# Kernel tuning notes

Hardware: AMD Instinct MI355X
Metric: run time of the kernel (lower is better)

## Reference

```python
import jax, jax.numpy as jnp
import numpy as np
import math

D_MODEL = 512
N_HEAD = 8
HEAD_DIM = D_MODEL // N_HEAD


def _rel_sinusoid(seq_len, dim):
    # Sinusoidal embedding for relative positions -seq_len .. seq_len-1, shape [2L, dim]
    half = dim // 2
    inv_freq = jnp.exp(jnp.arange(half, dtype=jnp.float32) * (-math.log(10000.0) / (half - 1)))
    ang = jnp.arange(-seq_len, seq_len, dtype=jnp.float32)[:, None] * inv_freq[None, :]
    return jnp.concatenate([jnp.sin(ang), jnp.cos(ang)], axis=1)  # [2L, dim]


def _shift(BD):
    # Transformer-XL shift trick: [b, n, L, 2L] -> [b, n, L, L]
    b, n, L, _ = BD.shape
    BD = jnp.concatenate([BD, jnp.zeros((b, n, L, 1), BD.dtype)], axis=-1)  # [b,n,L,2L+1]
    BD = BD.reshape(b, n, -1, L)[:, :, :-1].reshape(b, n, L, -1)  # [b,n,L,2L]
    return BD[:, :, :, L:]


def setup_inputs() -> dict:
    key = jax.random.key(0)
    ks = jax.random.split(key, 6)
    B, L = 8, 1024
    x = jax.random.normal(ks[0], (B, L, D_MODEL), jnp.float32)
    mask = jax.random.randint(ks[1], (B, L), 0, 2).astype(jnp.int32)
    W_qkv = jax.random.normal(ks[2], (D_MODEL, 3 * D_MODEL), jnp.float32) / math.sqrt(D_MODEL)
    r_r_bias = jax.random.normal(ks[3], (N_HEAD, HEAD_DIM), jnp.float32) * 0.1
    r_w_bias = jax.random.normal(ks[4], (N_HEAD, HEAD_DIM), jnp.float32) * 0.1
    w_kr = jax.random.normal(ks[5], (HEAD_DIM, HEAD_DIM), jnp.float32) * 0.1
    return {"x": x, "mask": mask, "W_qkv": W_qkv, "r_r_bias": r_r_bias, "r_w_bias": r_w_bias, "w_kr": w_kr}


def reference(x, mask, W_qkv, r_r_bias, r_w_bias, w_kr):
    B, L, d_model = x.shape
    scale = math.sqrt(HEAD_DIM)
    pos_embed = _rel_sinusoid(L, HEAD_DIM)  # [2L, head_dim]

    qkv = x @ W_qkv  # [B, L, 3*d_model]
    q, k, v = jnp.split(qkv, 3, axis=-1)
    q = q.reshape(B, L, N_HEAD, HEAD_DIM).transpose(0, 2, 1, 3)  # [B, H, L, hd]
    k = k.reshape(B, L, N_HEAD, HEAD_DIM).transpose(0, 2, 1, 3)
    v = v.reshape(B, L, N_HEAD, HEAD_DIM).transpose(0, 2, 1, 3)

    rw_head_q = q + r_r_bias[None, :, None, :]
    AC = jnp.einsum('bnqd,bnkd->bnqk', rw_head_q, k)  # [B,H,L,L]

    rel = pos_embed @ w_kr  # [2L, hd]
    D_ = jnp.einsum('nd,ld->nl', r_w_bias, rel)[None, :, None, :]  # [1,H,1,2L]
    B_ = jnp.einsum('bnqd,ld->bnql', q, rel)  # [B,H,L,2L]
    BD = _shift(B_ + D_)  # [B,H,L,L]

    attn = (AC + BD) / scale
    attn = jnp.where(mask[:, None, None, :] == 0, jnp.float32(1e-9), attn)
    attn = jax.nn.softmax(attn, axis=-1)  # dropout is identity at eval

    out = jnp.einsum('bnqk,bnkd->bnqd', attn, v)  # [B,H,L,hd]
    return out.transpose(0, 2, 1, 3).reshape(B, L, d_model)
```

## Files before the change

kernel.cpp:

```cpp
#include <hip/hip_runtime.h>
#include <hip/hip_bf16.h>
#include <stdint.h>

typedef __bf16 bf16x8 __attribute__((ext_vector_type(8)));
typedef float  f32x4  __attribute__((ext_vector_type(4)));

#define D_MODEL 512
#define N_HEAD  8
#define HD      64
#define L_      1024
#define SCALE   0.125f
#define EXP_NEG8 3.35462628e-4f
#define L2E     1.44269504f
#define NEG8L2E -11.54156036f

__device__ __forceinline__ unsigned short f2bf(float f) {
  unsigned int u = __builtin_bit_cast(unsigned int, f);
  u += 0x7FFFu + ((u >> 16) & 1u);
  return (unsigned short)(u >> 16);
}
__device__ __forceinline__ float bf2f(unsigned short h) {
  unsigned int u = ((unsigned int)h) << 16;
  return __builtin_bit_cast(float, u);
}

__device__ __forceinline__ void gld_lds16(const void* g, void* l) {
  __builtin_amdgcn_global_load_lds(
      (const __attribute__((address_space(1))) void*)g,
      (__attribute__((address_space(3))) void*)l, 16, 0, 0);
}
__device__ __forceinline__ void gld_lds4(const void* g, void* l) {
  __builtin_amdgcn_global_load_lds(
      (const __attribute__((address_space(1))) void*)g,
      (__attribute__((address_space(3))) void*)l, 4, 0, 0);
}

__global__ __launch_bounds__(256) void k_cvt_x(const float* __restrict__ x,
                                               unsigned short* __restrict__ xbf) {
  int t = blockIdx.x * 256 + threadIdx.x;
  const float4* p = reinterpret_cast<const float4*>(x) + (size_t)t * 2;
  float4 a = p[0], b = p[1];
  ushort4 o0 = { f2bf(a.x), f2bf(a.y), f2bf(a.z), f2bf(a.w) };
  ushort4 o1 = { f2bf(b.x), f2bf(b.y), f2bf(b.z), f2bf(b.w) };
  ushort4* q = reinterpret_cast<ushort4*>(xbf) + (size_t)t * 2;
  q[0] = o0; q[1] = o1;
}

__global__ __launch_bounds__(256) void k_cvt_wt(const float* __restrict__ W,
                                                unsigned short* __restrict__ Wt) {
  __shared__ float tile[32][33];
  int kb = blockIdx.x;
  int nb = blockIdx.y;
  int t = threadIdx.x;
  int r = t >> 3, c4 = (t & 7) * 4;
  float4 v = *reinterpret_cast<const float4*>(W + (size_t)(kb * 32 + r) * 1536 + nb * 32 + c4);
  tile[r][c4 + 0] = v.x; tile[r][c4 + 1] = v.y; tile[r][c4 + 2] = v.z; tile[r][c4 + 3] = v.w;
  __syncthreads();
  int a = t >> 3, b4 = (t & 7) * 4;
  ushort4 o = { f2bf(tile[b4 + 0][a]), f2bf(tile[b4 + 1][a]),
                f2bf(tile[b4 + 2][a]), f2bf(tile[b4 + 3][a]) };
  *reinterpret_cast<ushort4*>(Wt + (size_t)(nb * 32 + a) * 512 + kb * 32 + b4) = o;
}

__global__ __launch_bounds__(256) void k_stab(float* __restrict__ SCF,
                                              unsigned short* __restrict__ SBF) {
  int tid = blockIdx.x * 256 + threadIdx.x;
  int l = tid >> 6, d = tid & 63;
  const float kInv = -9.210340371976184f / 31.0f;
  float f = expf((float)(d & 31) * kInv);
  float ang = (float)l * f;
  float v = (d < 32) ? sinf(ang) : cosf(ang);
  SCF[tid] = v;
  SBF[tid] = f2bf(v);
}

__global__ __launch_bounds__(256) void k_wz(const unsigned short* __restrict__ Wt,
                                            const float* __restrict__ wkr,
                                            const float* __restrict__ rwb,
                                            unsigned short* __restrict__ Wzt,
                                            float* __restrict__ CZ) {
  __shared__ float wkrS[64][64];
  __shared__ float panS[64][36];
  int blk = blockIdx.x;
  int h = blk >> 4, kc = blk & 15;
  int t = threadIdx.x;
  for (int i = t; i < 4096; i += 256) wkrS[i >> 6][i & 63] = wkr[i];
  {
    int d = t >> 2, j0 = (t & 3) * 8;
    const unsigned short* src = Wt + (size_t)(h * 64 + d) * 512 + kc * 32 + j0;
    for (int j = 0; j < 8; ++j) panS[d][j0 + j] = bf2f(src[j]);
  }
  __syncthreads();
  int e = t >> 2, j0 = (t & 3) * 8;
  float acc[8];
  for (int j = 0; j < 8; ++j) acc[j] = 0.f;
  for (int d = 0; d < 64; ++d) {
    float wv = wkrS[e][d];
    for (int j = 0; j < 8; ++j) acc[j] += wv * panS[d][j0 + j];
  }
  unsigned short* dst = Wzt + (size_t)(h * 64 + e) * 512 + kc * 32 + j0;
  ushort4 o0 = { f2bf(acc[0]), f2bf(acc[1]), f2bf(acc[2]), f2bf(acc[3]) };
  ushort4 o1 = { f2bf(acc[4]), f2bf(acc[5]), f2bf(acc[6]), f2bf(acc[7]) };
  *reinterpret_cast<ushort4*>(dst) = o0;
  *reinterpret_cast<ushort4*>(dst + 4) = o1;
  if (kc == 0 && t < 64) {
    float c = 0.f;
    for (int d = 0; d < 64; ++d) c += wkrS[t][d] * rwb[h * 64 + d];
    CZ[h * 64 + t] = c;
  }
}

__global__ __launch_bounds__(256, 3) void k_gemm_qkv(const unsigned short* __restrict__ Xbf,
                                                     const unsigned short* __restrict__ Wt,
                                                     const float* __restrict__ rrb,
                                                     const float* __restrict__ SCF,
                                                     const float* __restrict__ CZ,
                                                     unsigned short* __restrict__ QKV,
                                                     unsigned short* __restrict__ Vt,
                                                     unsigned short* __restrict__ Aq) {
  __shared__ unsigned short As[2][128][32];
  __shared__ unsigned short Bs[2][128][32];
  int lin = blockIdx.y * 64 + blockIdx.x;
  int xcd = lin & 7, idx = lin >> 3;
  int bx = xcd * 8 + idx / 16;
  int by = idx % 16;
  int m0 = bx * 128;
  int n0 = by * 128;
  int w = threadIdx.x >> 6, lane = threadIdx.x & 63;
  int lr = lane & 15, g = lane >> 4;
  int wm = (w >> 1) * 64, wn = (w & 1) * 64;
  int srow = lane >> 2, schk = (lane & 3) * 8;

  auto stage = [&](int buf, int k0) {
#pragma unroll
    for (int j = 0; j < 2; ++j) {
      int row = w * 32 + j * 16 + srow;
      gld_lds16(Xbf + (size_t)(m0 + row) * 512 + k0 + schk, &As[buf][w * 32 + j * 16][0]);
      gld_lds16(Wt  + (size_t)(n0 + row) * 512 + k0 + schk, &Bs[buf][w * 32 + j * 16][0]);
    }
  };

  f32x4 acc[4][4];
  for (int i = 0; i < 4; ++i) for (int j = 0; j < 4; ++j) acc[i][j] = (f32x4){0.f, 0.f, 0.f, 0.f};

  stage(0, 0);
  __syncthreads();

  for (int it = 0; it < 16; ++it) {
    int cur = it & 1;
    if (it < 15) stage(cur ^ 1, (it + 1) * 32);
    bf16x8 a[4], b[4];
#pragma unroll
    for (int mt = 0; mt < 4; ++mt)
      a[mt] = __builtin_bit_cast(bf16x8, *reinterpret_cast<const uint4*>(&As[cur][wm + mt * 16 + lr][g * 8]));
#pragma unroll
    for (int nt = 0; nt < 4; ++nt)
      b[nt] = __builtin_bit_cast(bf16x8, *reinterpret_cast<const uint4*>(&Bs[cur][wn + nt * 16 + lr][g * 8]));
#pragma unroll
    for (int mt = 0; mt < 4; ++mt)
#pragma unroll
      for (int nt = 0; nt < 4; ++nt)
        acc[mt][nt] = __builtin_amdgcn_mfma_f32_16x16x32_bf16(a[mt], b[nt], acc[mt][nt], 0, 0, 0);
    __syncthreads();
  }

  int region = n0 >> 9;
  if (region == 3) {
    int nvb = (n0 - 1536) + wn;
    int h = nvb >> 6;
    int bb = m0 >> 10;
    float cz0 = CZ[nvb + lr];
    float cz1 = CZ[nvb + 16 + lr];
    float cz2 = CZ[nvb + 32 + lr];
    float cz3 = CZ[nvb + 48 + lr];
#pragma unroll
    for (int mt = 0; mt < 4; ++mt)
#pragma unroll
      for (int r = 0; r < 4; ++r) {
        int m = m0 + wm + mt * 16 + g * 4 + r;
        int lrow = m & 1023;
        const float* sc = SCF + (size_t)lrow * 64;
        float s0 = sc[lr], s1 = sc[16 + lr], c0 = sc[32 + lr], c1 = sc[48 + lr];
        float z0 = acc[mt][0][r] + cz0;
        float z1 = acc[mt][1][r] + cz1;
        float z2 = acc[mt][2][r] + cz2;
        float z3 = acc[mt][3][r] + cz3;
        unsigned short* ap = Aq + ((size_t)(bb * 8 + h) * 1024 + lrow) * 64;
        ap[lr]      = f2bf((z0 * c0 + z2 * s0) * SCALE);
        ap[16 + lr] = f2bf((z1 * c1 + z3 * s1) * SCALE);
        ap[32 + lr] = f2bf((z2 * c0 - z0 * s0) * SCALE);
        ap[48 + lr] = f2bf((z3 * c1 - z1 * s1) * SCALE);
      }
  } else if (region == 2) {
#pragma unroll
    for (int mt = 0; mt < 4; ++mt)
#pragma unroll
      for (int nt = 0; nt < 4; ++nt) {
        int m = m0 + wm + mt * 16 + g * 4;
        int n = n0 + wn + nt * 16 + lr;
        int nv = n - 1024;
        int bb = m >> 10, h = nv >> 6, d = nv & 63;
        ushort4 o = { f2bf(acc[mt][nt][0]), f2bf(acc[mt][nt][1]),
                      f2bf(acc[mt][nt][2]), f2bf(acc[mt][nt][3]) };
        *reinterpret_cast<ushort4*>(Vt + (size_t)((bb * 8 + h) * 64 + d) * 1024 + (m & 1023)) = o;
      }
  } else if (region == 0) {
#pragma unroll
    for (int mt = 0; mt < 4; ++mt)
#pragma unroll
      for (int nt = 0; nt < 4; ++nt) {
        int n = n0 + wn + nt * 16 + lr;
        float bias = rrb[n];
#pragma unroll
        for (int r = 0; r < 4; ++r) {
          int m = m0 + wm + mt * 16 + g * 4 + r;
          QKV[(size_t)m * 1536 + n] = f2bf((acc[mt][nt][r] + bias) * SCALE);
        }
      }
  } else {
#pragma unroll
    for (int mt = 0; mt < 4; ++mt)
#pragma unroll
      for (int nt = 0; nt < 4; ++nt)
#pragma unroll
        for (int r = 0; r < 4; ++r) {
          int m = m0 + wm + mt * 16 + g * 4 + r;
          int n = n0 + wn + nt * 16 + lr;
          QKV[(size_t)m * 1536 + n] = f2bf(acc[mt][nt][r]);
        }
  }
}

__global__ __launch_bounds__(256, 3) void k_attn(const unsigned short* __restrict__ QKV,
                                                 const unsigned short* __restrict__ Vt,
                                                 const unsigned short* __restrict__ Sbf,
                                                 const unsigned short* __restrict__ Aq,
                                                 const int* __restrict__ mask,
                                                 float* __restrict__ out) {
  __shared__ unsigned short KtS[2][64][64];
  __shared__ unsigned short VtS[2][64][64];
  __shared__ int MtS[2][64];
  __shared__ unsigned short pS[4][32][64];

  int n_ = blockIdx.x;
  int l = (n_ & 7) * 64 + (n_ >> 3);
  int bh = l >> 3, qt = l & 7;
  int b = bh >> 3, h = bh & 7;
  int w = threadIdx.x >> 6, lane = threadIdx.x & 63;
  int lr = lane & 15, g = lane >> 4;
  int qw0 = qt * 128 + w * 32;
  int rsub = lane >> 3;
  int csub = (lane & 7) ^ rsub;
  int swz = lr & 7;

  bf16x8 qrr[2][2], qa[2][2];
#pragma unroll
  for (int mt = 0; mt < 2; ++mt) {
    const unsigned short* qrow = QKV + (size_t)(b * L_ + qw0 + mt * 16 + lr) * 1536 + h * HD;
    const unsigned short* arow = Aq + ((size_t)bh * L_ + qw0 + mt * 16 + lr) * HD;
#pragma unroll
    for (int ks = 0; ks < 2; ++ks) {
      qrr[mt][ks] = __builtin_bit_cast(bf16x8, *reinterpret_cast<const uint4*>(qrow + ks * 32 + g * 8));
      qa[mt][ks]  = __builtin_bit_cast(bf16x8, *reinterpret_cast<const uint4*>(arow + ks * 32 + g * 8));
    }
  }

  auto stage = [&](int nb, int k0n) {
#pragma unroll
    for (int j = 0; j < 2; ++j) {
      int row = w * 16 + j * 8;
      const unsigned short* gK = QKV + (size_t)(b * L_ + k0n + row + rsub) * 1536 +
                                 D_MODEL + h * HD + csub * 8;
      gld_lds16(gK, &KtS[nb][row][0]);
      const unsigned short* gV = Vt + (size_t)(bh * HD + row + rsub) * L_ + k0n + csub * 8;
      gld_lds16(gV, &VtS[nb][row][0]);
    }
    if (w == 0) gld_lds4(mask + b * L_ + k0n + lane, &MtS[nb][0]);
  };

  stage(0, 0);

  float lsum[2] = {0.f, 0.f};
  f32x4 accO[2][4];
#pragma unroll
  for (int mt = 0; mt < 2; ++mt)
#pragma unroll
    for (int nt = 0; nt < 4; ++nt) accO[mt][nt] = (f32x4){0.f, 0.f, 0.f, 0.f};

  char* psw = (char*)&pS[w][0][0];
  __syncthreads();

  for (int it = 0; it < 16; ++it) {
    int k0 = it << 6;
    int cur = it & 1;
    if (it < 15) stage(cur ^ 1, k0 + 64);

    bf16x8 sf[4][2];
#pragma unroll
    for (int t4 = 0; t4 < 4; ++t4)
#pragma unroll
      for (int ks = 0; ks < 2; ++ks)
        sf[t4][ks] = __builtin_bit_cast(bf16x8, *reinterpret_cast<const uint4*>(
            Sbf + (size_t)(k0 + t4 * 16 + lr) * HD + ks * 32 + g * 8));

    f32x4 ac[2][4];
#pragma unroll
    for (int mt = 0; mt < 2; ++mt)
#pragma unroll
      for (int t4 = 0; t4 < 4; ++t4) ac[mt][t4] = (f32x4){0.f, 0.f, 0.f, 0.f};
#pragma unroll
    for (int t4 = 0; t4 < 4; ++t4) {
#pragma unroll
      for (int ks = 0; ks < 2; ++ks) {
        const unsigned short* kp = &KtS[cur][t4 * 16 + lr][((((ks << 2) | g) ^ swz) << 3)];
        bf16x8 kfr = __builtin_bit_cast(bf16x8, *reinterpret_cast<const uint4*>(kp));
        ac[0][t4] = __builtin_amdgcn_mfma_f32_16x16x32_bf16(kfr, qrr[0][ks], ac[0][t4], 0, 0, 0);
        ac[1][t4] = __builtin_amdgcn_mfma_f32_16x16x32_bf16(kfr, qrr[1][ks], ac[1][t4], 0, 0, 0);
      }
#pragma unroll
      for (int ks = 0; ks < 2; ++ks) {
        ac[0][t4] = __builtin_amdgcn_mfma_f32_16x16x32_bf16(sf[t4][ks], qa[0][ks], ac[0][t4], 0, 0, 0);
        ac[1][t4] = __builtin_amdgcn_mfma_f32_16x16x32_bf16(sf[t4][ks], qa[1][ks], ac[1][t4], 0, 0, 0);
      }
    }

#pragma unroll
    for (int t4 = 0; t4 < 4; ++t4) {
      int4 mk = *reinterpret_cast<const int4*>(&MtS[cur][t4 * 16 + g * 4]);
#pragma unroll
      for (int mt = 0; mt < 2; ++mt) {
        float e0 = __builtin_amdgcn_exp2f(fmaf(ac[mt][t4][0], L2E, NEG8L2E));
        float e1 = __builtin_amdgcn_exp2f(fmaf(ac[mt][t4][1], L2E, NEG8L2E));
        float e2 = __builtin_amdgcn_exp2f(fmaf(ac[mt][t4][2], L2E, NEG8L2E));
        float e3 = __builtin_amdgcn_exp2f(fmaf(ac[mt][t4][3], L2E, NEG8L2E));
        e0 = mk.x ? e0 : EXP_NEG8;
        e1 = mk.y ? e1 : EXP_NEG8;
        e2 = mk.z ? e2 : EXP_NEG8;
        e3 = mk.w ? e3 : EXP_NEG8;
        lsum[mt] += (e0 + e1) + (e2 + e3);
        unsigned int lo, hi;
        asm("v_cvt_pk_bf16_f32 %0, %1, %2" : "=v"(lo) : "v"(e0), "v"(e1));
        asm("v_cvt_pk_bf16_f32 %0, %1, %2" : "=v"(hi) : "v"(e2), "v"(e3));
        uint2 pk; pk.x = lo; pk.y = hi;
        *reinterpret_cast<uint2*>(psw + ((mt * 16 + lr) * 128 +
            (((t4 << 5) | (g << 3)) ^ (swz << 4)))) = pk;
      }
    }

    bf16x8 pa[2][2];
#pragma unroll
    for (int mt = 0; mt < 2; ++mt)
#pragma unroll
      for (int ks = 0; ks < 2; ++ks)
        pa[mt][ks] = __builtin_bit_cast(bf16x8, *reinterpret_cast<const uint4*>(
            psw + ((mt * 16 + lr) * 128 + (((ks << 6) | (g << 4)) ^ (swz << 4)))));
#pragma unroll
    for (int nt = 0; nt < 4; ++nt)
#pragma unroll
      for (int ks = 0; ks < 2; ++ks) {
        const unsigned short* vp = &VtS[cur][nt * 16 + lr][((((ks << 2) | g) ^ swz) << 3)];
        bf16x8 vfr = __builtin_bit_cast(bf16x8, *reinterpret_cast<const uint4*>(vp));
        accO[0][nt] = __builtin_amdgcn_mfma_f32_16x16x32_bf16(pa[0][ks], vfr, accO[0][nt], 0, 0, 0);
        accO[1][nt] = __builtin_amdgcn_mfma_f32_16x16x32_bf16(pa[1][ks], vfr, accO[1][nt], 0, 0, 0);
      }
    __syncthreads();
  }

#pragma unroll
  for (int mt = 0; mt < 2; ++mt) {
    lsum[mt] += __shfl_xor(lsum[mt], 16);
    lsum[mt] += __shfl_xor(lsum[mt], 32);
  }
  float dsum[2][4];
#pragma unroll
  for (int mt = 0; mt < 2; ++mt)
#pragma unroll
    for (int r = 0; r < 4; ++r) dsum[mt][r] = __shfl(lsum[mt], g * 4 + r);

#pragma unroll
  for (int mt = 0; mt < 2; ++mt)
#pragma unroll
    for (int nt = 0; nt < 4; ++nt)
#pragma unroll
      for (int r = 0; r < 4; ++r) {
        int q = qw0 + mt * 16 + g * 4 + r;
        out[(size_t)(b * L_ + q) * D_MODEL + h * HD + nt * 16 + lr] = accO[mt][nt][r] / dsum[mt][r];
      }
}

extern "C" void kernel_launch(void* const* d_in, const int* in_sizes, int n_in,
                              void* d_out, int out_size, void* d_ws, size_t ws_size,
                              hipStream_t stream) {
  const float* x    = (const float*)d_in[0];
  const int*   mask = (const int*)d_in[1];
  const float* Wqkv = (const float*)d_in[2];
  const float* rrb  = (const float*)d_in[3];
  const float* rwb  = (const float*)d_in[4];
  const float* wkr  = (const float*)d_in[5];
  float* out = (float*)d_out;

  char* ws = (char*)d_ws;
  size_t off = 0;
  unsigned short* XBF = (unsigned short*)(ws + off); off += (size_t)8192 * 512 * 2;
  unsigned short* WT  = (unsigned short*)(ws + off); off += (size_t)2048 * 512 * 2;
  unsigned short* QKV = (unsigned short*)(ws + off); off += (size_t)8192 * 1536 * 2;
  unsigned short* VT  = (unsigned short*)(ws + off); off += (size_t)64 * 64 * 1024 * 2;
  unsigned short* AQ  = (unsigned short*)(ws + off); off += (size_t)64 * 1024 * 64 * 2;
  float*          SCF = (float*)(ws + off);          off += (size_t)1024 * 64 * 4;
  unsigned short* SBF = (unsigned short*)(ws + off); off += (size_t)1024 * 64 * 2;
  float*          CZ  = (float*)(ws + off);          off += 512 * 4;

  hipLaunchKernelGGL(k_cvt_x,    dim3(2048),   dim3(256), 0, stream, x, XBF);
  hipLaunchKernelGGL(k_cvt_wt,   dim3(16, 48), dim3(256), 0, stream, Wqkv, WT);
  hipLaunchKernelGGL(k_stab,     dim3(256),    dim3(256), 0, stream, SCF, SBF);
  hipLaunchKernelGGL(k_wz,       dim3(128),    dim3(256), 0, stream, WT, wkr, rwb, WT + (size_t)1536 * 512, CZ);
  hipLaunchKernelGGL(k_gemm_qkv, dim3(64, 16), dim3(256), 0, stream, XBF, WT, rrb, SCF, CZ, QKV, VT, AQ);
  hipLaunchKernelGGL(k_attn,     dim3(512),    dim3(256), 0, stream, QKV, VT, SBF, AQ, mask, out);
}
```

Measured before the change: 92.75 us.

## Fuse x conversion into QKV GEMM and software-pipeline the attention PV stage

Drops the separate fp32-to-bf16 kernel for x. The QKV GEMM now loads fp32 x into registers, converts it and writes it to LDS while the previous tile's MFMAs run. In attention, the PV matmul for tile it-1 is deferred into iteration it using a triple-buffered V tile, and the S-table and mask loads move from LDS staging to register prefetch. This removes a kernel launch and a round trip of x through global memory, and overlaps softmax with MFMA, at the cost of more registers (launch bounds lowered from 3 to 2 blocks per SM for attention).

After: 115.3 us. +24.3%, slower.

```diff
diff --git a/kernel.cpp b/kernel.cpp
--- a/kernel.cpp
+++ b/kernel.cpp
@@ -28,22 +28,6 @@
   __builtin_amdgcn_global_load_lds(
       (const __attribute__((address_space(1))) void*)g,
       (__attribute__((address_space(3))) void*)l, 16, 0, 0);
-}
-__device__ __forceinline__ void gld_lds4(const void* g, void* l) {
-  __builtin_amdgcn_global_load_lds(
-      (const __attribute__((address_space(1))) void*)g,
-      (__attribute__((address_space(3))) void*)l, 4, 0, 0);
-}
-
-__global__ __launch_bounds__(256) void k_cvt_x(const float* __restrict__ x,
-                                               unsigned short* __restrict__ xbf) {
-  int t = blockIdx.x * 256 + threadIdx.x;
-  const float4* p = reinterpret_cast<const float4*>(x) + (size_t)t * 2;
-  float4 a = p[0], b = p[1];
-  ushort4 o0 = { f2bf(a.x), f2bf(a.y), f2bf(a.z), f2bf(a.w) };
-  ushort4 o1 = { f2bf(b.x), f2bf(b.y), f2bf(b.z), f2bf(b.w) };
-  ushort4* q = reinterpret_cast<ushort4*>(xbf) + (size_t)t * 2;
-  q[0] = o0; q[1] = o1;
 }
 
 __global__ __launch_bounds__(256) void k_cvt_wt(const float* __restrict__ W,
@@ -110,7 +94,7 @@
   }
 }
 
-__global__ __launch_bounds__(256, 3) void k_gemm_qkv(const unsigned short* __restrict__ Xbf,
+__global__ __launch_bounds__(256, 3) void k_gemm_qkv(const float* __restrict__ Xf,
                                                      const unsigned short* __restrict__ Wt,
                                                      const float* __restrict__ rrb,
                                                      const float* __restrict__ SCF,
@@ -130,39 +114,60 @@
   int lr = lane & 15, g = lane >> 4;
   int wm = (w >> 1) * 64, wn = (w & 1) * 64;
   int srow = lane >> 2, schk = (lane & 3) * 8;
-
-  auto stage = [&](int buf, int k0) {
+  int a_r = lane >> 3, a_c4 = (lane & 7) * 4;
+
+  auto loadA = [&](int k0, float4 (&fr)[4]) {
+#pragma unroll
+    for (int j = 0; j < 4; ++j)
+      fr[j] = *reinterpret_cast<const float4*>(
+          Xf + (size_t)(m0 + w * 32 + j * 8 + a_r) * 512 + k0 + a_c4);
+  };
+  auto writeA = [&](int buf, float4 (&fr)[4]) {
+#pragma unroll
+    for (int j = 0; j < 4; ++j) {
+      unsigned int u0, u1;
+      asm("v_cvt_pk_bf16_f32 %0, %1, %2" : "=v"(u0) : "v"(fr[j].x), "v"(fr[j].y));
+      asm("v_cvt_pk_bf16_f32 %0, %1, %2" : "=v"(u1) : "v"(fr[j].z), "v"(fr[j].w));
+      uint2 pk2; pk2.x = u0; pk2.y = u1;
+      *reinterpret_cast<uint2*>(&As[buf][w * 32 + j * 8 + a_r][a_c4]) = pk2;
+    }
+  };
+  auto stageB = [&](int buf, int k0) {
 #pragma unroll
     for (int j = 0; j < 2; ++j) {
       int row = w * 32 + j * 16 + srow;
-      gld_lds16(Xbf + (size_t)(m0 + row) * 512 + k0 + schk, &As[buf][w * 32 + j * 16][0]);
-      gld_lds16(Wt  + (size_t)(n0 + row) * 512 + k0 + schk, &Bs[buf][w * 32 + j * 16][0]);
+      gld_lds16(Wt + (size_t)(n0 + row) * 512 + k0 + schk, &Bs[buf][w * 32 + j * 16][0]);
     }
   };
 
   f32x4 acc[4][4];
   for (int i = 0; i < 4; ++i) for (int j = 0; j < 4; ++j) acc[i][j] = (f32x4){0.f, 0.f, 0.f, 0.f};
 
-  stage(0, 0);
+  float4 fA[4], fB[4];
+  loadA(0, fA);
+  stageB(0, 0);
+  writeA(0, fA);
   __syncthreads();
 
-  for (int it = 0; it < 16; ++it) {
-    int cur = it & 1;
-    if (it < 15) stage(cur ^ 1, (it + 1) * 32);
-    bf16x8 a[4], b[4];
-#pragma unroll
-    for (int mt = 0; mt < 4; ++mt)
-      a[mt] = __builtin_bit_cast(bf16x8, *reinterpret_cast<const uint4*>(&As[cur][wm + mt * 16 + lr][g * 8]));
+  auto step = [&](int it, float4 (&curR)[4], float4 (&nxtR)[4]) {
+    int cb = it & 1;
+    if (it < 15) { loadA((it + 1) * 32, nxtR); stageB(cb ^ 1, (it + 1) * 32); }
+    bf16x8 a[4], b2[4];
+#pragma unroll
+    for (int mt = 0; mt < 4; ++mt)
+      a[mt] = __builtin_bit_cast(bf16x8, *reinterpret_cast<const uint4*>(&As[cb][wm + mt * 16 + lr][g * 8]));
 #pragma unroll
     for (int nt = 0; nt < 4; ++nt)
-      b[nt] = __builtin_bit_cast(bf16x8, *reinterpret_cast<const uint4*>(&Bs[cur][wn + nt * 16 + lr][g * 8]));
+      b2[nt] = __builtin_bit_cast(bf16x8, *reinterpret_cast<const uint4*>(&Bs[cb][wn + nt * 16 + lr][g * 8]));
 #pragma unroll
     for (int mt = 0; mt < 4; ++mt)
 #pragma unroll
       for (int nt = 0; nt < 4; ++nt)
-        acc[mt][nt] = __builtin_amdgcn_mfma_f32_16x16x32_bf16(a[mt], b[nt], acc[mt][nt], 0, 0, 0);
+        acc[mt][nt] = __builtin_amdgcn_mfma_f32_16x16x32_bf16(a[mt], b2[nt], acc[mt][nt], 0, 0, 0);
+    if (it < 15) writeA(cb ^ 1, nxtR);
     __syncthreads();
-  }
+  };
+  for (int base = 0; base < 16; base += 2) { step(base, fA, fB); step(base + 1, fB, fA); }
 
   int region = n0 >> 9;
   if (region == 3) {
@@ -231,15 +236,14 @@
   }
 }
 
-__global__ __launch_bounds__(256, 3) void k_attn(const unsigned short* __restrict__ QKV,
+__global__ __launch_bounds__(256, 2) void k_attn(const unsigned short* __restrict__ QKV,
                                                  const unsigned short* __restrict__ Vt,
                                                  const unsigned short* __restrict__ Sbf,
                                                  const unsigned short* __restrict__ Aq,
                                                  const int* __restrict__ mask,
                                                  float* __restrict__ out) {
   __shared__ unsigned short KtS[2][64][64];
-  __shared__ unsigned short VtS[2][64][64];
-  __shared__ int MtS[2][64];
+  __shared__ unsigned short VtS[3][64][64];
   __shared__ unsigned short pS[4][32][64];
 
   int n_ = blockIdx.x;
@@ -265,20 +269,28 @@
     }
   }
 
-  auto stage = [&](int nb, int k0n) {
-#pragma unroll
-    for (int j = 0; j < 2; ++j) {
-      int row = w * 16 + j * 8;
+  auto stage = [&](int j) {
+    int kb = j & 1, vb = j % 3;
+    int k0n = j << 6;
+#pragma unroll
+    for (int jj = 0; jj < 2; ++jj) {
+      int row = w * 16 + jj * 8;
       const unsigned short* gK = QKV + (size_t)(b * L_ + k0n + row + rsub) * 1536 +
                                  D_MODEL + h * HD + csub * 8;
-      gld_lds16(gK, &KtS[nb][row][0]);
+      gld_lds16(gK, &KtS[kb][row][0]);
       const unsigned short* gV = Vt + (size_t)(bh * HD + row + rsub) * L_ + k0n + csub * 8;
-      gld_lds16(gV, &VtS[nb][row][0]);
-    }
-    if (w == 0) gld_lds4(mask + b * L_ + k0n + lane, &MtS[nb][0]);
-  };
-
-  stage(0, 0);
+      gld_lds16(gV, &VtS[vb][row][0]);
+    }
+  };
+  auto loadSF = [&](int j, bf16x8 (&sf)[4][2]) {
+    int k0n = j << 6;
+#pragma unroll
+    for (int t4 = 0; t4 < 4; ++t4)
+#pragma unroll
+      for (int ks = 0; ks < 2; ++ks)
+        sf[t4][ks] = __builtin_bit_cast(bf16x8, *reinterpret_cast<const uint4*>(
+            Sbf + (size_t)(k0n + t4 * 16 + lr) * HD + ks * 32 + g * 8));
+  };
 
   float lsum[2] = {0.f, 0.f};
   f32x4 accO[2][4];
@@ -288,20 +300,21 @@
     for (int nt = 0; nt < 4; ++nt) accO[mt][nt] = (f32x4){0.f, 0.f, 0.f, 0.f};
 
   char* psw = (char*)&pS[w][0][0];
+
+  bf16x8 sfA[4][2], sfB[4][2];
+  stage(0);
+  loadSF(0, sfA);
   __syncthreads();
 
-  for (int it = 0; it < 16; ++it) {
+  auto iter = [&](int it, bf16x8 (&sfC)[4][2], bf16x8 (&sfN)[4][2]) {
     int k0 = it << 6;
-    int cur = it & 1;
-    if (it < 15) stage(cur ^ 1, k0 + 64);
-
-    bf16x8 sf[4][2];
+    int kb = it & 1;
+    if (it < 15) { stage(it + 1); loadSF(it + 1, sfN); }
+
+    int4 mk[4];
 #pragma unroll
     for (int t4 = 0; t4 < 4; ++t4)
-#pragma unroll
-      for (int ks = 0; ks < 2; ++ks)
-        sf[t4][ks] = __builtin_bit_cast(bf16x8, *reinterpret_cast<const uint4*>(
-            Sbf + (size_t)(k0 + t4 * 16 + lr) * HD + ks * 32 + g * 8));
+      mk[t4] = *reinterpret_cast<const int4*>(mask + b * L_ + k0 + t4 * 16 + g * 4);
 
     f32x4 ac[2][4];
 #pragma unroll
@@ -312,31 +325,48 @@
     for (int t4 = 0; t4 < 4; ++t4) {
 #pragma unroll
       for (int ks = 0; ks < 2; ++ks) {
-        const unsigned short* kp = &KtS[cur][t4 * 16 + lr][((((ks << 2) | g) ^ swz) << 3)];
+        const unsigned short* kp = &KtS[kb][t4 * 16 + lr][((((ks << 2) | g) ^ swz) << 3)];
         bf16x8 kfr = __builtin_bit_cast(bf16x8, *reinterpret_cast<const uint4*>(kp));
         ac[0][t4] = __builtin_amdgcn_mfma_f32_16x16x32_bf16(kfr, qrr[0][ks], ac[0][t4], 0, 0, 0);
         ac[1][t4] = __builtin_amdgcn_mfma_f32_16x16x32_bf16(kfr, qrr[1][ks], ac[1][t4], 0, 0, 0);
       }
 #pragma unroll
       for (int ks = 0; ks < 2; ++ks) {
-        ac[0][t4] = __builtin_amdgcn_mfma_f32_16x16x32_bf16(sf[t4][ks], qa[0][ks], ac[0][t4], 0, 0, 0);
-        ac[1][t4] = __builtin_amdgcn_mfma_f32_16x16x32_bf16(sf[t4][ks], qa[1][ks], ac[1][t4], 0, 0, 0);
-      }
+        ac[0][t4] = __builtin_amdgcn_mfma_f32_16x16x32_bf16(sfC[t4][ks], qa[0][ks], ac[0][t4], 0, 0, 0);
+        ac[1][t4] = __builtin_amdgcn_mfma_f32_16x16x32_bf16(sfC[t4][ks], qa[1][ks], ac[1][t4], 0, 0, 0);
+      }
+    }
+
+    bf16x8 pa[2][2], vfr[4][2];
+    if (it > 0) {
+      int vbp = (it - 1) % 3;
+#pragma unroll
+      for (int mt = 0; mt < 2; ++mt)
+#pragma unroll
+        for (int ks = 0; ks < 2; ++ks)
+          pa[mt][ks] = __builtin_bit_cast(bf16x8, *reinterpret_cast<const uint4*>(
+              psw + ((mt * 16 + lr) * 128 + (((ks << 6) | (g << 4)) ^ (swz << 4)))));
+#pragma unroll
+      for (int nt = 0; nt < 4; ++nt)
+#pragma unroll
+        for (int ks = 0; ks < 2; ++ks) {
+          const unsigned short* vp = &VtS[vbp][nt * 16 + lr][((((ks << 2) | g) ^ swz) << 3)];
+          vfr[nt][ks] = __builtin_bit_cast(bf16x8, *reinterpret_cast<const uint4*>(vp));
+        }
     }
 
 #pragma unroll
     for (int t4 = 0; t4 < 4; ++t4) {
-      int4 mk = *reinterpret_cast<const int4*>(&MtS[cur][t4 * 16 + g * 4]);
 #pragma unroll
       for (int mt = 0; mt < 2; ++mt) {
         float e0 = __builtin_amdgcn_exp2f(fmaf(ac[mt][t4][0], L2E, NEG8L2E));
         float e1 = __builtin_amdgcn_exp2f(fmaf(ac[mt][t4][1], L2E, NEG8L2E));
         float e2 = __builtin_amdgcn_exp2f(fmaf(ac[mt][t4][2], L2E, NEG8L2E));
         float e3 = __builtin_amdgcn_exp2f(fmaf(ac[mt][t4][3], L2E, NEG8L2E));
-        e0 = mk.x ? e0 : EXP_NEG8;
-        e1 = mk.y ? e1 : EXP_NEG8;
-        e2 = mk.z ? e2 : EXP_NEG8;
-        e3 = mk.w ? e3 : EXP_NEG8;
+        e0 = mk[t4].x ? e0 : EXP_NEG8;
+        e1 = mk[t4].y ? e1 : EXP_NEG8;
+        e2 = mk[t4].z ? e2 : EXP_NEG8;
+        e3 = mk[t4].w ? e3 : EXP_NEG8;
         lsum[mt] += (e0 + e1) + (e2 + e3);
         unsigned int lo, hi;
         asm("v_cvt_pk_bf16_f32 %0, %1, %2" : "=v"(lo) : "v"(e0), "v"(e1));
@@ -347,6 +377,24 @@
       }
     }
 
+    if (it > 0) {
+#pragma unroll
+      for (int nt = 0; nt < 4; ++nt)
+#pragma unroll
+        for (int ks = 0; ks < 2; ++ks) {
+          accO[0][nt] = __builtin_amdgcn_mfma_f32_16x16x32_bf16(pa[0][ks], vfr[nt][ks], accO[0][nt], 0, 0, 0);
+          accO[1][nt] = __builtin_amdgcn_mfma_f32_16x16x32_bf16(pa[1][ks], vfr[nt][ks], accO[1][nt], 0, 0, 0);
+        }
+    }
+    __syncthreads();
+  };
+
+  for (int base = 0; base < 16; base += 2) {
+    iter(base, sfA, sfB);
+    iter(base + 1, sfB, sfA);
+  }
+
+  {
     bf16x8 pa[2][2];
 #pragma unroll
     for (int mt = 0; mt < 2; ++mt)
@@ -358,12 +406,11 @@
     for (int nt = 0; nt < 4; ++nt)
 #pragma unroll
       for (int ks = 0; ks < 2; ++ks) {
-        const unsigned short* vp = &VtS[cur][nt * 16 + lr][((((ks << 2) | g) ^ swz) << 3)];
+        const unsigned short* vp = &VtS[0][nt * 16 + lr][((((ks << 2) | g) ^ swz) << 3)];
         bf16x8 vfr = __builtin_bit_cast(bf16x8, *reinterpret_cast<const uint4*>(vp));
         accO[0][nt] = __builtin_amdgcn_mfma_f32_16x16x32_bf16(pa[0][ks], vfr, accO[0][nt], 0, 0, 0);
         accO[1][nt] = __builtin_amdgcn_mfma_f32_16x16x32_bf16(pa[1][ks], vfr, accO[1][nt], 0, 0, 0);
       }
-    __syncthreads();
   }
 
 #pragma unroll
@@ -401,7 +448,6 @@
 
   char* ws = (char*)d_ws;
   size_t off = 0;
-  unsigned short* XBF = (unsigned short*)(ws + off); off += (size_t)8192 * 512 * 2;
   unsigned short* WT  = (unsigned short*)(ws + off); off += (size_t)2048 * 512 * 2;
   unsigned short* QKV = (unsigned short*)(ws + off); off += (size_t)8192 * 1536 * 2;
   unsigned short* VT  = (unsigned short*)(ws + off); off += (size_t)64 * 64 * 1024 * 2;
@@ -410,10 +456,9 @@
   unsigned short* SBF = (unsigned short*)(ws + off); off += (size_t)1024 * 64 * 2;
   float*          CZ  = (float*)(ws + off);          off += 512 * 4;
 
-  hipLaunchKernelGGL(k_cvt_x,    dim3(2048),   dim3(256), 0, stream, x, XBF);
   hipLaunchKernelGGL(k_cvt_wt,   dim3(16, 48), dim3(256), 0, stream, Wqkv, WT);
   hipLaunchKernelGGL(k_stab,     dim3(256),    dim3(256), 0, stream, SCF, SBF);
   hipLaunchKernelGGL(k_wz,       dim3(128),    dim3(256), 0, stream, WT, wkr, rwb, WT + (size_t)1536 * 512, CZ);
-  hipLaunchKernelGGL(k_gemm_qkv, dim3(64, 16), dim3(256), 0, stream, XBF, WT, rrb, SCF, CZ, QKV, VT, AQ);
+  hipLaunchKernelGGL(k_gemm_qkv, dim3(64, 16), dim3(256), 0, stream, x, WT, rrb, SCF, CZ, QKV, VT, AQ);
   hipLaunchKernelGGL(k_attn,     dim3(512),    dim3(256), 0, stream, QKV, VT, SBF, AQ, mask, out);
 }
```

## Use 8 waves per attention block with 16 query rows each, add setprio

Applied to the files above, without the earlier changes.

The attention kernel now launches 512 threads per block. Each of the 8 waves handles 16 query rows instead of 32, so the per-wave accumulator and fragment state is halved. K/V staging is split across more waves, and s_setprio raises wave priority around the MFMA sections. This adds more waves per CU to hide latency. In exchange, each wave reuses its K/V LDS fragment reads over fewer query rows, so LDS traffic per FLOP doubles.

New measurement: 116.8 us. 25.9% more time.

```diff
diff --git a/kernel.cpp b/kernel.cpp
--- a/kernel.cpp
+++ b/kernel.cpp
@@ -231,7 +231,7 @@
   }
 }
 
-__global__ __launch_bounds__(256, 3) void k_attn(const unsigned short* __restrict__ QKV,
+__global__ __launch_bounds__(512, 2) void k_attn(const unsigned short* __restrict__ QKV,
                                                  const unsigned short* __restrict__ Vt,
                                                  const unsigned short* __restrict__ Sbf,
                                                  const unsigned short* __restrict__ Aq,
@@ -240,7 +240,7 @@
   __shared__ unsigned short KtS[2][64][64];
   __shared__ unsigned short VtS[2][64][64];
   __shared__ int MtS[2][64];
-  __shared__ unsigned short pS[4][32][64];
+  __shared__ unsigned short pS[8][16][64];
 
   int n_ = blockIdx.x;
   int l = (n_ & 7) * 64 + (n_ >> 3);
@@ -248,44 +248,38 @@
   int b = bh >> 3, h = bh & 7;
   int w = threadIdx.x >> 6, lane = threadIdx.x & 63;
   int lr = lane & 15, g = lane >> 4;
-  int qw0 = qt * 128 + w * 32;
+  int qw0 = qt * 128 + w * 16;
   int rsub = lane >> 3;
   int csub = (lane & 7) ^ rsub;
   int swz = lr & 7;
 
-  bf16x8 qrr[2][2], qa[2][2];
-#pragma unroll
-  for (int mt = 0; mt < 2; ++mt) {
-    const unsigned short* qrow = QKV + (size_t)(b * L_ + qw0 + mt * 16 + lr) * 1536 + h * HD;
-    const unsigned short* arow = Aq + ((size_t)bh * L_ + qw0 + mt * 16 + lr) * HD;
+  bf16x8 qrr[2], qa[2];
+  {
+    const unsigned short* qrow = QKV + (size_t)(b * L_ + qw0 + lr) * 1536 + h * HD;
+    const unsigned short* arow = Aq + ((size_t)bh * L_ + qw0 + lr) * HD;
 #pragma unroll
     for (int ks = 0; ks < 2; ++ks) {
-      qrr[mt][ks] = __builtin_bit_cast(bf16x8, *reinterpret_cast<const uint4*>(qrow + ks * 32 + g * 8));
-      qa[mt][ks]  = __builtin_bit_cast(bf16x8, *reinterpret_cast<const uint4*>(arow + ks * 32 + g * 8));
+      qrr[ks] = __builtin_bit_cast(bf16x8, *reinterpret_cast<const uint4*>(qrow + ks * 32 + g * 8));
+      qa[ks]  = __builtin_bit_cast(bf16x8, *reinterpret_cast<const uint4*>(arow + ks * 32 + g * 8));
     }
   }
 
   auto stage = [&](int nb, int k0n) {
-#pragma unroll
-    for (int j = 0; j < 2; ++j) {
-      int row = w * 16 + j * 8;
-      const unsigned short* gK = QKV + (size_t)(b * L_ + k0n + row + rsub) * 1536 +
-                                 D_MODEL + h * HD + csub * 8;
-      gld_lds16(gK, &KtS[nb][row][0]);
-      const unsigned short* gV = Vt + (size_t)(bh * HD + row + rsub) * L_ + k0n + csub * 8;
-      gld_lds16(gV, &VtS[nb][row][0]);
-    }
+    int row = w * 8;
+    const unsigned short* gK = QKV + (size_t)(b * L_ + k0n + row + rsub) * 1536 +
+                               D_MODEL + h * HD + csub * 8;
+    gld_lds16(gK, &KtS[nb][row][0]);
+    const unsigned short* gV = Vt + (size_t)(bh * HD + row + rsub) * L_ + k0n + csub * 8;
+    gld_lds16(gV, &VtS[nb][row][0]);
     if (w == 0) gld_lds4(mask + b * L_ + k0n + lane, &MtS[nb][0]);
   };
 
   stage(0, 0);
 
-  float lsum[2] = {0.f, 0.f};
-  f32x4 accO[2][4];
-#pragma unroll
-  for (int mt = 0; mt < 2; ++mt)
-#pragma unroll
-    for (int nt = 0; nt < 4; ++nt) accO[mt][nt] = (f32x4){0.f, 0.f, 0.f, 0.f};
+  float lsum = 0.f;
+  f32x4 accO[4];
+#pragma unroll
+  for (int nt = 0; nt < 4; ++nt) accO[nt] = (f32x4){0.f, 0.f, 0.f, 0.f};
 
   char* psw = (char*)&pS[w][0][0];
   __syncthreads();
@@ -303,89 +297,74 @@
         sf[t4][ks] = __builtin_bit_cast(bf16x8, *reinterpret_cast<const uint4*>(
             Sbf + (size_t)(k0 + t4 * 16 + lr) * HD + ks * 32 + g * 8));
 
-    f32x4 ac[2][4];
-#pragma unroll
-    for (int mt = 0; mt < 2; ++mt)
-#pragma unroll
-      for (int t4 = 0; t4 < 4; ++t4) ac[mt][t4] = (f32x4){0.f, 0.f, 0.f, 0.f};
+    f32x4 ac[4];
+#pragma unroll
+    for (int t4 = 0; t4 < 4; ++t4) ac[t4] = (f32x4){0.f, 0.f, 0.f, 0.f};
+    __builtin_amdgcn_s_setprio(1);
 #pragma unroll
     for (int t4 = 0; t4 < 4; ++t4) {
 #pragma unroll
       for (int ks = 0; ks < 2; ++ks) {
         const unsigned short* kp = &KtS[cur][t4 * 16 + lr][((((ks << 2) | g) ^ swz) << 3)];
         bf16x8 kfr = __builtin_bit_cast(bf16x8, *reinterpret_cast<const uint4*>(kp));
-        ac[0][t4] = __builtin_amdgcn_mfma_f32_16x16x32_bf16(kfr, qrr[0][ks], ac[0][t4], 0, 0, 0);
-        ac[1][t4] = __builtin_amdgcn_mfma_f32_16x16x32_bf16(kfr, qrr[1][ks], ac[1][t4], 0, 0, 0);
-      }
-#pragma unroll
-      for (int ks = 0; ks < 2; ++ks) {
-        ac[0][t4] = __builtin_amdgcn_mfma_f32_16x16x32_bf16(sf[t4][ks], qa[0][ks], ac[0][t4], 0, 0, 0);
-        ac[1][t4] = __builtin_amdgcn_mfma_f32_16x16x32_bf16(sf[t4][ks], qa[1][ks], ac[1][t4], 0, 0, 0);
-      }
-    }
+        ac[t4] = __builtin_amdgcn_mfma_f32_16x16x32_bf16(kfr, qrr[ks], ac[t4], 0, 0, 0);
+      }
+#pragma unroll
+      for (int ks = 0; ks < 2; ++ks)
+        ac[t4] = __builtin_amdgcn_mfma_f32_16x16x32_bf16(sf[t4][ks], qa[ks], ac[t4], 0, 0, 0);
+    }
+    __builtin_amdgcn_s_setprio(0);
 
 #pragma unroll
     for (int t4 = 0; t4 < 4; ++t4) {
       int4 mk = *reinterpret_cast<const int4*>(&MtS[cur][t4 * 16 + g * 4]);
-#pragma unroll
-      for (int mt = 0; mt < 2; ++mt) {
-        float e0 = __builtin_amdgcn_exp2f(fmaf(ac[mt][t4][0], L2E, NEG8L2E));
-        float e1 = __builtin_amdgcn_exp2f(fmaf(ac[mt][t4][1], L2E, NEG8L2E));
-        float e2 = __builtin_amdgcn_exp2f(fmaf(ac[mt][t4][2], L2E, NEG8L2E));
-        float e3 = __builtin_amdgcn_exp2f(fmaf(ac[mt][t4][3], L2E, NEG8L2E));
-        e0 = mk.x ? e0 : EXP_NEG8;
-        e1 = mk.y ? e1 : EXP_NEG8;
-        e2 = mk.z ? e2 : EXP_NEG8;
-        e3 = mk.w ? e3 : EXP_NEG8;
-        lsum[mt] += (e0 + e1) + (e2 + e3);
-        unsigned int lo, hi;
-        asm("v_cvt_pk_bf16_f32 %0, %1, %2" : "=v"(lo) : "v"(e0), "v"(e1));
-        asm("v_cvt_pk_bf16_f32 %0, %1, %2" : "=v"(hi) : "v"(e2), "v"(e3));
-        uint2 pk; pk.x = lo; pk.y = hi;
-        *reinterpret_cast<uint2*>(psw + ((mt * 16 + lr) * 128 +
-            (((t4 << 5) | (g << 3)) ^ (swz << 4)))) = pk;
-      }
-    }
-
-    bf16x8 pa[2][2];
-#pragma unroll
-    for (int mt = 0; mt < 2; ++mt)
-#pragma unroll
-      for (int ks = 0; ks < 2; ++ks)
-        pa[mt][ks] = __builtin_bit_cast(bf16x8, *reinterpret_cast<const uint4*>(
-            psw + ((mt * 16 + lr) * 128 + (((ks << 6) | (g << 4)) ^ (swz << 4)))));
+      float e0 = __builtin_amdgcn_exp2f(fmaf(ac[t4][0], L2E, NEG8L2E));
+      float e1 = __builtin_amdgcn_exp2f(fmaf(ac[t4][1], L2E, NEG8L2E));
+      float e2 = __builtin_amdgcn_exp2f(fmaf(ac[t4][2], L2E, NEG8L2E));
+      float e3 = __builtin_amdgcn_exp2f(fmaf(ac[t4][3], L2E, NEG8L2E));
+      e0 = mk.x ? e0 : EXP_NEG8;
+      e1 = mk.y ? e1 : EXP_NEG8;
+      e2 = mk.z ? e2 : EXP_NEG8;
+      e3 = mk.w ? e3 : EXP_NEG8;
+      lsum += (e0 + e1) + (e2 + e3);
+      unsigned int lo, hi;
+      asm("v_cvt_pk_bf16_f32 %0, %1, %2" : "=v"(lo) : "v"(e0), "v"(e1));
+      asm("v_cvt_pk_bf16_f32 %0, %1, %2" : "=v"(hi) : "v"(e2), "v"(e3));
+      uint2 pk; pk.x = lo; pk.y = hi;
+      *reinterpret_cast<uint2*>(psw + (lr * 128 + (((t4 << 5) | (g << 3)) ^ (swz << 4)))) = pk;
+    }
+
+    bf16x8 pa[2];
+#pragma unroll
+    for (int ks = 0; ks < 2; ++ks)
+      pa[ks] = __builtin_bit_cast(bf16x8, *reinterpret_cast<const uint4*>(
+          psw + (lr * 128 + (((ks << 6) | (g << 4)) ^ (swz << 4)))));
+    __builtin_amdgcn_s_setprio(1);
 #pragma unroll
     for (int nt = 0; nt < 4; ++nt)
 #pragma unroll
       for (int ks = 0; ks < 2; ++ks) {
         const unsigned short* vp = &VtS[cur][nt * 16 + lr][((((ks << 2) | g) ^ swz) << 3)];
         bf16x8 vfr = __builtin_bit_cast(bf16x8, *reinterpret_cast<const uint4*>(vp));
-        accO[0][nt] = __builtin_amdgcn_mfma_f32_16x16x32_bf16(pa[0][ks], vfr, accO[0][nt], 0, 0, 0);
-        accO[1][nt] = __builtin_amdgcn_mfma_f32_16x16x32_bf16(pa[1][ks], vfr, accO[1][nt], 0, 0, 0);
-      }
+        accO[nt] = __builtin_amdgcn_mfma_f32_16x16x32_bf16(pa[ks], vfr, accO[nt], 0, 0, 0);
+      }
+    __builtin_amdgcn_s_setprio(0);
     __syncthreads();
   }
 
-#pragma unroll
-  for (int mt = 0; mt < 2; ++mt) {
-    lsum[mt] += __shfl_xor(lsum[mt], 16);
-    lsum[mt] += __shfl_xor(lsum[mt], 32);
-  }
-  float dsum[2][4];
-#pragma unroll
-  for (int mt = 0; mt < 2; ++mt)
-#pragma unroll
-    for (int r = 0; r < 4; ++r) dsum[mt][r] = __shfl(lsum[mt], g * 4 + r);
-
-#pragma unroll
-  for (int mt = 0; mt < 2; ++mt)
-#pragma unroll
-    for (int nt = 0; nt < 4; ++nt)
-#pragma unroll
-      for (int r = 0; r < 4; ++r) {
-        int q = qw0 + mt * 16 + g * 4 + r;
-        out[(size_t)(b * L_ + q) * D_MODEL + h * HD + nt * 16 + lr] = accO[mt][nt][r] / dsum[mt][r];
-      }
+  lsum += __shfl_xor(lsum, 16);
+  lsum += __shfl_xor(lsum, 32);
+  float dsum[4];
+#pragma unroll
+  for (int r = 0; r < 4; ++r) dsum[r] = __shfl(lsum, g * 4 + r);
+
+#pragma unroll
+  for (int nt = 0; nt < 4; ++nt)
+#pragma unroll
+    for (int r = 0; r < 4; ++r) {
+      int q = qw0 + g * 4 + r;
+      out[(size_t)(b * L_ + q) * D_MODEL + h * HD + nt * 16 + lr] = accO[nt][r] / dsum[r];
+    }
 }
 
 extern "C" void kernel_launch(void* const* d_in, const int* in_sizes, int n_in,
@@ -415,5 +394,5 @@
   hipLaunchKernelGGL(k_stab,     dim3(256),    dim3(256), 0, stream, SCF, SBF);
   hipLaunchKernelGGL(k_wz,       dim3(128),    dim3(256), 0, stream, WT, wkr, rwb, WT + (size_t)1536 * 512, CZ);
   hipLaunchKernelGGL(k_gemm_qkv, dim3(64, 16), dim3(256), 0, stream, XBF, WT, rrb, SCF, CZ, QKV, VT, AQ);
-  hipLaunchKernelGGL(k_attn,     dim3(512),    dim3(256), 0, stream, QKV, VT, SBF, AQ, mask, out);
-}
+  hipLaunchKernelGGL(k_attn,     dim3(512),    dim3(512), 0, stream, QKV, VT, SBF, AQ, mask, out);
+}
```

## Stage 128-key K/V tiles per iteration and read mask directly from global

Applied to the files above, without the earlier changes.

The attention kernel now stages 128 keys of K and V per double-buffered step instead of 64, processing each step as two 64-key halves. This halves the number of block barriers and async staging rounds. V tiles get a new XOR-swizzled layout for the wider rows. The mask is no longer staged through LDS and is read per lane from global memory. Doubling the LDS tiles lowers the occupancy hint from 3 to 2 blocks per CU, which may reduce latency hiding.

Result: slower. 96.25 us (+3.8%).

```diff
diff --git a/kernel.cpp b/kernel.cpp
--- a/kernel.cpp
+++ b/kernel.cpp
@@ -28,11 +28,6 @@
   __builtin_amdgcn_global_load_lds(
       (const __attribute__((address_space(1))) void*)g,
       (__attribute__((address_space(3))) void*)l, 16, 0, 0);
-}
-__device__ __forceinline__ void gld_lds4(const void* g, void* l) {
-  __builtin_amdgcn_global_load_lds(
-      (const __attribute__((address_space(1))) void*)g,
-      (__attribute__((address_space(3))) void*)l, 4, 0, 0);
 }
 
 __global__ __launch_bounds__(256) void k_cvt_x(const float* __restrict__ x,
@@ -231,15 +226,14 @@
   }
 }
 
-__global__ __launch_bounds__(256, 3) void k_attn(const unsigned short* __restrict__ QKV,
+__global__ __launch_bounds__(256, 2) void k_attn(const unsigned short* __restrict__ QKV,
                                                  const unsigned short* __restrict__ Vt,
                                                  const unsigned short* __restrict__ Sbf,
                                                  const unsigned short* __restrict__ Aq,
                                                  const int* __restrict__ mask,
                                                  float* __restrict__ out) {
-  __shared__ unsigned short KtS[2][64][64];
-  __shared__ unsigned short VtS[2][64][64];
-  __shared__ int MtS[2][64];
+  __shared__ unsigned short KtS[2][128][64];
+  __shared__ unsigned short VtS[2][64][128];
   __shared__ unsigned short pS[4][32][64];
 
   int n_ = blockIdx.x;
@@ -251,6 +245,8 @@
   int qw0 = qt * 128 + w * 32;
   int rsub = lane >> 3;
   int csub = (lane & 7) ^ rsub;
+  int vrs = lane >> 4;
+  int vch = lane & 15;
   int swz = lr & 7;
 
   bf16x8 qrr[2][2], qa[2][2];
@@ -267,15 +263,19 @@
 
   auto stage = [&](int nb, int k0n) {
 #pragma unroll
-    for (int j = 0; j < 2; ++j) {
-      int row = w * 16 + j * 8;
+    for (int j = 0; j < 4; ++j) {
+      int row = w * 32 + j * 8;
       const unsigned short* gK = QKV + (size_t)(b * L_ + k0n + row + rsub) * 1536 +
                                  D_MODEL + h * HD + csub * 8;
       gld_lds16(gK, &KtS[nb][row][0]);
-      const unsigned short* gV = Vt + (size_t)(bh * HD + row + rsub) * L_ + k0n + csub * 8;
+    }
+#pragma unroll
+    for (int j = 0; j < 4; ++j) {
+      int row = w * 16 + j * 4;
+      int xorv = (row & 4) | vrs;
+      const unsigned short* gV = Vt + (size_t)(bh * HD + row + vrs) * L_ + k0n + ((vch ^ xorv) << 3);
       gld_lds16(gV, &VtS[nb][row][0]);
     }
-    if (w == 0) gld_lds4(mask + b * L_ + k0n + lane, &MtS[nb][0]);
   };
 
   stage(0, 0);
@@ -290,10 +290,9 @@
   char* psw = (char*)&pS[w][0][0];
   __syncthreads();
 
-  for (int it = 0; it < 16; ++it) {
-    int k0 = it << 6;
-    int cur = it & 1;
-    if (it < 15) stage(cur ^ 1, k0 + 64);
+  auto half = [&](int nb, int k0, int hh) {
+    int k0h = k0 + hh * 64;
+    int rbase = hh * 64;
 
     bf16x8 sf[4][2];
 #pragma unroll
@@ -301,7 +300,11 @@
 #pragma unroll
       for (int ks = 0; ks < 2; ++ks)
         sf[t4][ks] = __builtin_bit_cast(bf16x8, *reinterpret_cast<const uint4*>(
-            Sbf + (size_t)(k0 + t4 * 16 + lr) * HD + ks * 32 + g * 8));
+            Sbf + (size_t)(k0h + t4 * 16 + lr) * HD + ks * 32 + g * 8));
+    int4 mk[4];
+#pragma unroll
+    for (int t4 = 0; t4 < 4; ++t4)
+      mk[t4] = *reinterpret_cast<const int4*>(mask + b * L_ + k0h + t4 * 16 + g * 4);
 
     f32x4 ac[2][4];
 #pragma unroll
@@ -312,7 +315,7 @@
     for (int t4 = 0; t4 < 4; ++t4) {
 #pragma unroll
       for (int ks = 0; ks < 2; ++ks) {
-        const unsigned short* kp = &KtS[cur][t4 * 16 + lr][((((ks << 2) | g) ^ swz) << 3)];
+        const unsigned short* kp = &KtS[nb][rbase + t4 * 16 + lr][((((ks << 2) | g) ^ swz) << 3)];
         bf16x8 kfr = __builtin_bit_cast(bf16x8, *reinterpret_cast<const uint4*>(kp));
         ac[0][t4] = __builtin_amdgcn_mfma_f32_16x16x32_bf16(kfr, qrr[0][ks], ac[0][t4], 0, 0, 0);
         ac[1][t4] = __builtin_amdgcn_mfma_f32_16x16x32_bf16(kfr, qrr[1][ks], ac[1][t4], 0, 0, 0);
@@ -326,17 +329,16 @@
 
 #pragma unroll
     for (int t4 = 0; t4 < 4; ++t4) {
-      int4 mk = *reinterpret_cast<const int4*>(&MtS[cur][t4 * 16 + g * 4]);
 #pragma unroll
       for (int mt = 0; mt < 2; ++mt) {
         float e0 = __builtin_amdgcn_exp2f(fmaf(ac[mt][t4][0], L2E, NEG8L2E));
         float e1 = __builtin_amdgcn_exp2f(fmaf(ac[mt][t4][1], L2E, NEG8L2E));
         float e2 = __builtin_amdgcn_exp2f(fmaf(ac[mt][t4][2], L2E, NEG8L2E));
         float e3 = __builtin_amdgcn_exp2f(fmaf(ac[mt][t4][3], L2E, NEG8L2E));
-        e0 = mk.x ? e0 : EXP_NEG8;
-        e1 = mk.y ? e1 : EXP_NEG8;
-        e2 = mk.z ? e2 : EXP_NEG8;
-        e3 = mk.w ? e3 : EXP_NEG8;
+        e0 = mk[t4].x ? e0 : EXP_NEG8;
+        e1 = mk[t4].y ? e1 : EXP_NEG8;
+        e2 = mk[t4].z ? e2 : EXP_NEG8;
+        e3 = mk[t4].w ? e3 : EXP_NEG8;
         lsum[mt] += (e0 + e1) + (e2 + e3);
         unsigned int lo, hi;
         asm("v_cvt_pk_bf16_f32 %0, %1, %2" : "=v"(lo) : "v"(e0), "v"(e1));
@@ -358,11 +360,20 @@
     for (int nt = 0; nt < 4; ++nt)
 #pragma unroll
       for (int ks = 0; ks < 2; ++ks) {
-        const unsigned short* vp = &VtS[cur][nt * 16 + lr][((((ks << 2) | g) ^ swz) << 3)];
+        int chunk = (hh << 3) | (ks << 2) | g;
+        const unsigned short* vp = &VtS[nb][nt * 16 + lr][(chunk ^ swz) << 3];
         bf16x8 vfr = __builtin_bit_cast(bf16x8, *reinterpret_cast<const uint4*>(vp));
         accO[0][nt] = __builtin_amdgcn_mfma_f32_16x16x32_bf16(pa[0][ks], vfr, accO[0][nt], 0, 0, 0);
         accO[1][nt] = __builtin_amdgcn_mfma_f32_16x16x32_bf16(pa[1][ks], vfr, accO[1][nt], 0, 0, 0);
       }
+  };
+
+  for (int it = 0; it < 8; ++it) {
+    int k0 = it << 7;
+    int nb = it & 1;
+    if (it < 7) stage(nb ^ 1, k0 + 128);
+    half(nb, k0, 0);
+    half(nb, k0, 1);
     __syncthreads();
   }
 
```
